# Performance work log

Measured on AMD Instinct MI355X. Metric: run time of the kernel, lower is better.

## Reference

```python
import jax, jax.numpy as jnp
import numpy as np

EPS = 1e-8  # torch F.cosine_similarity denominator clamp


def setup_inputs() -> dict:
    key = jax.random.key(0)
    k1, k2 = jax.random.split(key)
    N, D = 8192, 256
    return {
        "output1": jax.random.normal(k1, (N, D), dtype=jnp.float32),
        "output2": jax.random.normal(k2, (N, D), dtype=jnp.float32),
    }


def reference(output1, output2):
    N = output2.shape[0]
    # cosine similarity matrix via normalize + GEMM, with torch's eps clamp
    n1 = jnp.linalg.norm(output1, axis=-1, keepdims=True)  # [N,1]
    n2 = jnp.linalg.norm(output2, axis=-1, keepdims=True)  # [N,1]
    dots = output1 @ output2.T  # [N,N]
    denom = jnp.maximum(n1 * n2.T, EPS)
    cos = dots / denom
    # subtract tiny diagonal as in original
    cos = cos - jnp.eye(N, dtype=cos.dtype) * 1e-12
    # cross entropy with labels = arange(N)
    logZ = jax.nn.logsumexp(cos, axis=-1)  # [N]
    diag = jnp.diagonal(cos)  # logits at true label i
    loss = jnp.mean(logZ - diag)
    return loss
```

## Files before the change

kernel.cpp:

```cpp
#include <hip/hip_runtime.h>
#include <hip/hip_bf16.h>

#define N 8192
#define D 256
#define SP 8
#define NCHK 16

typedef __bf16 bf16x8 __attribute__((ext_vector_type(8)));
typedef float f32x4 __attribute__((ext_vector_type(4)));

static __device__ __forceinline__ unsigned short f2bf(float x) {
    union { float f; unsigned int u; } c; c.f = x;
    unsigned int r = (c.u + 0x7fffu + ((c.u >> 16) & 1u)) >> 16;
    return (unsigned short)r;
}

static __device__ __forceinline__ void gll16(const void* g, void* l) {
    __builtin_amdgcn_global_load_lds(
        (const __attribute__((address_space(1))) void*)g,
        (__attribute__((address_space(3))) void*)l, 16, 0, 0);
}

#define WAIT_VM4  asm volatile("s_waitcnt vmcnt(4)" ::: "memory")
#define WAIT_VM0  asm volatile("s_waitcnt vmcnt(0)" ::: "memory")
#define WAIT_LG0  asm volatile("s_waitcnt lgkmcnt(0)" ::: "memory")
#define SBAR      __builtin_amdgcn_s_barrier()
#define SCHED0    __builtin_amdgcn_sched_barrier(0)

__global__ __launch_bounds__(256) void conv_k(const float* __restrict__ o1,
                                              const float* __restrict__ o2,
                                              unsigned char* __restrict__ a_bf,
                                              unsigned char* __restrict__ b_bf,
                                              float* __restrict__ diag) {
    const int wid = threadIdx.x >> 6, lane = threadIdx.x & 63;
    const int r = blockIdx.x * 4 + wid;
    const float4* p1 = (const float4*)(o1 + (size_t)r * D);
    const float4* p2 = (const float4*)(o2 + (size_t)r * D);
    float4 v1 = p1[lane], v2 = p2[lane];
    float s1 = v1.x*v1.x + v1.y*v1.y + v1.z*v1.z + v1.w*v1.w;
    float s2 = v2.x*v2.x + v2.y*v2.y + v2.z*v2.z + v2.w*v2.w;
    float sd = v1.x*v2.x + v1.y*v2.y + v1.z*v2.z + v1.w*v2.w;
    #pragma unroll
    for (int m = 1; m < 64; m <<= 1) {
        s1 += __shfl_xor(s1, m);
        s2 += __shfl_xor(s2, m);
        sd += __shfl_xor(sd, m);
    }
    float i1 = 1.0f / sqrtf(s1);
    float i2 = 1.0f / sqrtf(s2);
    if (lane == 0) diag[r] = sd * i1 * i2;

    {
        unsigned int lo = (unsigned int)f2bf(v1.x * i1) | ((unsigned int)f2bf(v1.y * i1) << 16);
        unsigned int hi = (unsigned int)f2bf(v1.z * i1) | ((unsigned int)f2bf(v1.w * i1) << 16);
        uint2 q; q.x = lo; q.y = hi;
        *(uint2*)(a_bf + (size_t)r * 512 + lane * 8) = q;
    }
    {
        unsigned int lo = (unsigned int)f2bf(v2.x * i2) | ((unsigned int)f2bf(v2.y * i2) << 16);
        unsigned int hi = (unsigned int)f2bf(v2.z * i2) | ((unsigned int)f2bf(v2.w * i2) << 16);
        int c  = lane >> 1;
        int cs = c ^ (r & 31);
        uint2 q; q.x = lo; q.y = hi;
        *(uint2*)(b_bf + (size_t)r * 512 + cs * 16 + (lane & 1) * 8) = q;
    }
}

__global__ __launch_bounds__(512, 2) void gemm7(const unsigned char* __restrict__ a_bf,
                                                const unsigned char* __restrict__ b_bf,
                                                float* __restrict__ s_part) {
    __shared__ __align__(16) unsigned char bls[3][64 * 512];
    __shared__ float red[2][256];

    const int tid = threadIdx.x;
    const int lane = tid & 63, wid = tid >> 6;
    const int wr = wid >> 1, wc = wid & 1;
    const int l15 = lane & 15, lk = lane >> 4;
    const int bid = blockIdx.x;
    const int sp = bid & 7, rb = bid >> 3;

    const unsigned char* aG = a_bf + (size_t)rb * (256 * 512);
    const unsigned char* bG = b_bf + (size_t)sp * ((size_t)1024 * 512);

    bf16x8 af[4][8];
    #pragma unroll
    for (int mr = 0; mr < 4; ++mr)
        #pragma unroll
        for (int ks = 0; ks < 8; ++ks)
            af[mr][ks] = *(const bf16x8*)(aG + (size_t)(wr * 64 + mr * 16 + l15) * 512
                                             + ks * 64 + lk * 16);

    #pragma unroll
    for (int it = 0; it < 4; ++it) {
        int x = it * 8192 + tid * 16;
        gll16(bG + x, &bls[0][x]);
    }
    #pragma unroll
    for (int it = 0; it < 4; ++it) {
        int x = it * 8192 + tid * 16;
        gll16(bG + 32768 + x, &bls[1][x]);
    }

    float srow[4][4];
    #pragma unroll
    for (int mr = 0; mr < 4; ++mr)
        #pragma unroll
        for (int rg = 0; rg < 4; ++rg) srow[mr][rg] = 0.f;

    const unsigned char* cur = bls[0];
    const unsigned char* nx1 = bls[1];
    const unsigned char* stg = bls[2];

    #pragma unroll 1
    for (int p = 0; p < NCHK; ++p) {
        if (p < NCHK - 1) { WAIT_VM4; } else { WAIT_VM0; }
        SCHED0;
        SBAR;

        if (p < NCHK - 2) {
            const unsigned char* src = bG + (size_t)(p + 2) * 32768;
            #pragma unroll
            for (int it = 0; it < 4; ++it) {
                int x = it * 8192 + tid * 16;
                gll16(src + x, (unsigned char*)stg + x);
            }
        }

        f32x4 acc[4][2];
        #pragma unroll
        for (int mr = 0; mr < 4; ++mr)
            #pragma unroll
            for (int nc = 0; nc < 2; ++nc)
                acc[mr][nc] = (f32x4){0.f, 0.f, 0.f, 0.f};

        __builtin_amdgcn_s_setprio(1);
        #pragma unroll
        for (int ks = 0; ks < 8; ++ks) {
            bf16x8 bb[2];
            #pragma unroll
            for (int nc = 0; nc < 2; ++nc) {
                const int col = wc * 32 + nc * 16 + l15;
                const int cs = (ks * 4 + lk) ^ (col & 31);
                bb[nc] = *(const bf16x8*)(cur + col * 512 + cs * 16);
            }
            #pragma unroll
            for (int nc = 0; nc < 2; ++nc)
                #pragma unroll
                for (int mr = 0; mr < 4; ++mr)
                    acc[mr][nc] = __builtin_amdgcn_mfma_f32_16x16x32_bf16(
                        af[mr][ks], bb[nc], acc[mr][nc], 0, 0, 0);
        }
        __builtin_amdgcn_s_setprio(0);
        WAIT_LG0;
        SCHED0;

        #pragma unroll
        for (int mr = 0; mr < 4; ++mr)
            #pragma unroll
            for (int rg = 0; rg < 4; ++rg)
                srow[mr][rg] += __expf(acc[mr][0][rg]) + __expf(acc[mr][1][rg]);

        const unsigned char* t = cur; cur = nx1; nx1 = stg; stg = t;
    }

    #pragma unroll
    for (int mr = 0; mr < 4; ++mr)
        #pragma unroll
        for (int rg = 0; rg < 4; ++rg) {
            float v = srow[mr][rg];
            v += __shfl_xor(v, 1);
            v += __shfl_xor(v, 2);
            v += __shfl_xor(v, 4);
            v += __shfl_xor(v, 8);
            srow[mr][rg] = v;
        }
    if (l15 == 0) {
        #pragma unroll
        for (int mr = 0; mr < 4; ++mr)
            #pragma unroll
            for (int rg = 0; rg < 4; ++rg)
                red[wc][wr * 64 + mr * 16 + lk * 4 + rg] = srow[mr][rg];
    }
    __syncthreads();
    if (tid < 256) {
        s_part[(size_t)sp * N + rb * 256 + tid] = red[0][tid] + red[1][tid];
    }
}

__global__ __launch_bounds__(128) void rowloss3(const float* __restrict__ s_part,
                                                const float* __restrict__ diag,
                                                float* __restrict__ partial) {
    const int t = threadIdx.x, rb = blockIdx.x;
    float s = 0.f;
    #pragma unroll
    for (int sp = 0; sp < SP; ++sp)
        s += s_part[(size_t)sp * N + rb * 128 + t];
    float loss = logf(s) - diag[rb * 128 + t];
    #pragma unroll
    for (int m = 1; m < 64; m <<= 1) loss += __shfl_xor(loss, m);
    __shared__ float redl[2];
    if ((t & 63) == 0) redl[t >> 6] = loss;
    __syncthreads();
    if (t == 0) partial[rb] = redl[0] + redl[1];
}

__global__ __launch_bounds__(64) void final_k(const float* __restrict__ partial,
                                              float* __restrict__ out) {
    const int t = threadIdx.x;
    float v = partial[t];
    #pragma unroll
    for (int m = 1; m < 64; m <<= 1) v += __shfl_xor(v, m);
    if (t == 0) out[0] = v / (float)N;
}

extern "C" void kernel_launch(void* const* d_in, const int* in_sizes, int n_in,
                              void* d_out, int out_size, void* d_ws, size_t ws_size,
                              hipStream_t stream) {
    const float* o1 = (const float*)d_in[0];
    const float* o2 = (const float*)d_in[1];

    unsigned char* w = (unsigned char*)d_ws;
    unsigned char* a_bf = w;
    unsigned char* b_bf = w + (size_t)4 * 1024 * 1024;
    float* diag    = (float*)(w + (size_t)8 * 1024 * 1024);
    float* s_part  = diag + N;
    float* partial = s_part + (size_t)SP * N;

    conv_k<<<N / 4, 256, 0, stream>>>(o1, o2, a_bf, b_bf, diag);
    gemm7<<<256, 512, 0, stream>>>(a_bf, b_bf, s_part);
    rowloss3<<<N / 128, 128, 0, stream>>>(s_part, diag, partial);
    final_k<<<1, 64, 0, stream>>>(partial, (float*)d_out);
}
```

Measured before the change: 53.16 us.

## Double-buffer B with interleaved prefetch and fold log2e into A for exp2

Replaces the triple-buffered B pipeline (prefetch two chunks ahead) with a double buffer. Loads for the next chunk are issued in four slices interleaved with the MFMA quarters, and barriers sit between the quarters. The A operand is pre-scaled by log2(e) during conversion so the softmax sum can use exp2f instead of __expf. Launch bounds drop from 2 to 1 block per CU, which frees registers but lowers occupancy. The extra barriers and the single chunk of lookahead may leave more memory latency exposed than the previous schedule did.

```diff
diff --git a/kernel.cpp b/kernel.cpp
--- a/kernel.cpp
+++ b/kernel.cpp
@@ -4,7 +4,8 @@
 #define N 8192
 #define D 256
 #define SP 8
-#define NCHK 16
+#define NCH 16
+#define LOG2E 1.44269504088896f
 
 typedef __bf16 bf16x8 __attribute__((ext_vector_type(8)));
 typedef float f32x4 __attribute__((ext_vector_type(4)));
@@ -21,7 +22,6 @@
         (__attribute__((address_space(3))) void*)l, 16, 0, 0);
 }
 
-#define WAIT_VM4  asm volatile("s_waitcnt vmcnt(4)" ::: "memory")
 #define WAIT_VM0  asm volatile("s_waitcnt vmcnt(0)" ::: "memory")
 #define WAIT_LG0  asm volatile("s_waitcnt lgkmcnt(0)" ::: "memory")
 #define SBAR      __builtin_amdgcn_s_barrier()
@@ -50,9 +50,10 @@
     float i2 = 1.0f / sqrtf(s2);
     if (lane == 0) diag[r] = sd * i1 * i2;
 
+    float a_sc = i1 * LOG2E;
     {
-        unsigned int lo = (unsigned int)f2bf(v1.x * i1) | ((unsigned int)f2bf(v1.y * i1) << 16);
-        unsigned int hi = (unsigned int)f2bf(v1.z * i1) | ((unsigned int)f2bf(v1.w * i1) << 16);
+        unsigned int lo = (unsigned int)f2bf(v1.x * a_sc) | ((unsigned int)f2bf(v1.y * a_sc) << 16);
+        unsigned int hi = (unsigned int)f2bf(v1.z * a_sc) | ((unsigned int)f2bf(v1.w * a_sc) << 16);
         uint2 q; q.x = lo; q.y = hi;
         *(uint2*)(a_bf + (size_t)r * 512 + lane * 8) = q;
     }
@@ -66,10 +67,10 @@
     }
 }
 
-__global__ __launch_bounds__(512, 2) void gemm7(const unsigned char* __restrict__ a_bf,
-                                                const unsigned char* __restrict__ b_bf,
-                                                float* __restrict__ s_part) {
-    __shared__ __align__(16) unsigned char bls[3][64 * 512];
+__global__ __launch_bounds__(512, 1) void gemm10(const unsigned char* __restrict__ a_bf,
+                                                 const unsigned char* __restrict__ b_bf,
+                                                 float* __restrict__ s_part) {
+    __shared__ __align__(16) unsigned char bls[2][32768];
     __shared__ float red[2][256];
 
     const int tid = threadIdx.x;
@@ -77,10 +78,10 @@
     const int wr = wid >> 1, wc = wid & 1;
     const int l15 = lane & 15, lk = lane >> 4;
     const int bid = blockIdx.x;
-    const int sp = bid & 7, rb = bid >> 3;
+    const int panel = bid & 7, rb = bid >> 3;
 
     const unsigned char* aG = a_bf + (size_t)rb * (256 * 512);
-    const unsigned char* bG = b_bf + (size_t)sp * ((size_t)1024 * 512);
+    const unsigned char* bG = b_bf + (size_t)panel * ((size_t)1024 * 512);
 
     bf16x8 af[4][8];
     #pragma unroll
@@ -95,11 +96,6 @@
         int x = it * 8192 + tid * 16;
         gll16(bG + x, &bls[0][x]);
     }
-    #pragma unroll
-    for (int it = 0; it < 4; ++it) {
-        int x = it * 8192 + tid * 16;
-        gll16(bG + 32768 + x, &bls[1][x]);
-    }
 
     float srow[4][4];
     #pragma unroll
@@ -107,24 +103,12 @@
         #pragma unroll
         for (int rg = 0; rg < 4; ++rg) srow[mr][rg] = 0.f;
 
-    const unsigned char* cur = bls[0];
-    const unsigned char* nx1 = bls[1];
-    const unsigned char* stg = bls[2];
+    int cur = 0;
 
     #pragma unroll 1
-    for (int p = 0; p < NCHK; ++p) {
-        if (p < NCHK - 1) { WAIT_VM4; } else { WAIT_VM0; }
-        SCHED0;
+    for (int p = 0; p < NCH; ++p) {
+        WAIT_VM0; SCHED0;
         SBAR;
-
-        if (p < NCHK - 2) {
-            const unsigned char* src = bG + (size_t)(p + 2) * 32768;
-            #pragma unroll
-            for (int it = 0; it < 4; ++it) {
-                int x = it * 8192 + tid * 16;
-                gll16(src + x, (unsigned char*)stg + x);
-            }
-        }
 
         f32x4 acc[4][2];
         #pragma unroll
@@ -133,34 +117,47 @@
             for (int nc = 0; nc < 2; ++nc)
                 acc[mr][nc] = (f32x4){0.f, 0.f, 0.f, 0.f};
 
-        __builtin_amdgcn_s_setprio(1);
-        #pragma unroll
-        for (int ks = 0; ks < 8; ++ks) {
-            bf16x8 bb[2];
-            #pragma unroll
-            for (int nc = 0; nc < 2; ++nc) {
-                const int col = wc * 32 + nc * 16 + l15;
-                const int cs = (ks * 4 + lk) ^ (col & 31);
-                bb[nc] = *(const bf16x8*)(cur + col * 512 + cs * 16);
+        const unsigned char* cb = bls[cur];
+        unsigned char* nb = bls[cur ^ 1];
+
+        #pragma unroll
+        for (int q = 0; q < 4; ++q) {
+            bf16x8 bb[2][2];
+            #pragma unroll
+            for (int dk = 0; dk < 2; ++dk)
+                #pragma unroll
+                for (int nc = 0; nc < 2; ++nc) {
+                    const int ks = 2 * q + dk;
+                    const int col = wc * 32 + nc * 16 + l15;
+                    const int cs = (ks * 4 + lk) ^ (col & 31);
+                    bb[dk][nc] = *(const bf16x8*)(cb + col * 512 + cs * 16);
+                }
+            if (p < NCH - 1) {
+                int x = q * 8192 + tid * 16;
+                gll16(bG + (size_t)(p + 1) * 32768 + x, nb + x);
             }
-            #pragma unroll
-            for (int nc = 0; nc < 2; ++nc)
+            SBAR;
+            WAIT_LG0; SCHED0;
+            __builtin_amdgcn_s_setprio(1);
+            #pragma unroll
+            for (int dk = 0; dk < 2; ++dk)
                 #pragma unroll
-                for (int mr = 0; mr < 4; ++mr)
-                    acc[mr][nc] = __builtin_amdgcn_mfma_f32_16x16x32_bf16(
-                        af[mr][ks], bb[nc], acc[mr][nc], 0, 0, 0);
+                for (int nc = 0; nc < 2; ++nc)
+                    #pragma unroll
+                    for (int mr = 0; mr < 4; ++mr)
+                        acc[mr][nc] = __builtin_amdgcn_mfma_f32_16x16x32_bf16(
+                            af[mr][2 * q + dk], bb[dk][nc], acc[mr][nc], 0, 0, 0);
+            __builtin_amdgcn_s_setprio(0);
+            if (q < 3) SBAR;
         }
-        __builtin_amdgcn_s_setprio(0);
-        WAIT_LG0;
-        SCHED0;
 
         #pragma unroll
         for (int mr = 0; mr < 4; ++mr)
             #pragma unroll
             for (int rg = 0; rg < 4; ++rg)
-                srow[mr][rg] += __expf(acc[mr][0][rg]) + __expf(acc[mr][1][rg]);
-
-        const unsigned char* t = cur; cur = nx1; nx1 = stg; stg = t;
+                srow[mr][rg] += exp2f(acc[mr][0][rg]) + exp2f(acc[mr][1][rg]);
+
+        cur ^= 1;
     }
 
     #pragma unroll
@@ -183,7 +180,7 @@
     }
     __syncthreads();
     if (tid < 256) {
-        s_part[(size_t)sp * N + rb * 256 + tid] = red[0][tid] + red[1][tid];
+        s_part[(size_t)panel * N + rb * 256 + tid] = red[0][tid] + red[1][tid];
     }
 }
 
@@ -227,7 +224,7 @@
     float* partial = s_part + (size_t)SP * N;
 
     conv_k<<<N / 4, 256, 0, stream>>>(o1, o2, a_bf, b_bf, diag);
-    gemm7<<<256, 512, 0, stream>>>(a_bf, b_bf, s_part);
+    gemm10<<<256, 512, 0, stream>>>(a_bf, b_bf, s_part);
     rowloss3<<<N / 128, 128, 0, stream>>>(s_part, diag, partial);
     final_k<<<1, 64, 0, stream>>>(partial, (float*)d_out);
 }
```

Result: slower. 60.57 us (+13.9%).
